# Kernel optimization log

Measured on AMD Instinct MI355X. Metric: run time of the kernel, lower is better.

## Reference

```python
import jax, jax.numpy as jnp
import numpy as np

N_NODES = 100000
N_EDGES = 1600000
IN_CH, OUT_CH = 6, 32


def _glorot(key, shape):
    fan_in, fan_out = shape[0], shape[1]
    lim = float(np.sqrt(6.0 / (fan_in + fan_out)))
    return jax.random.uniform(key, shape, jnp.float32, -lim, lim)


def setup_inputs() -> dict:
    key = jax.random.key(0)
    ks = jax.random.split(key, 16)
    x = jax.random.normal(ks[0], (N_NODES, IN_CH), jnp.float32)
    edge_tp = jax.random.randint(ks[1], (2, N_EDGES), 0, N_NODES, jnp.int32)
    edge_int = jax.random.randint(ks[2], (2, N_EDGES), 0, N_NODES, jnp.int32)
    return {
        'x': x, 'edge_tp': edge_tp, 'edge_int': edge_int,
        # block 1 (6 -> 32): self lin, per-edge-type message lins, residual proj
        'W_self1': _glorot(ks[3], (IN_CH, OUT_CH)), 'b1': jnp.zeros((OUT_CH,), jnp.float32),
        'W_tp1': _glorot(ks[4], (IN_CH, OUT_CH)), 'W_int1': _glorot(ks[5], (IN_CH, OUT_CH)),
        'W_res1': _glorot(ks[6], (IN_CH, OUT_CH)),
        # block 2 (32 -> 32): identity residual
        'W_self2': _glorot(ks[7], (OUT_CH, OUT_CH)), 'b2': jnp.zeros((OUT_CH,), jnp.float32),
        'W_tp2': _glorot(ks[8], (OUT_CH, OUT_CH)), 'W_int2': _glorot(ks[9], (OUT_CH, OUT_CH)),
        # instance decoder MLP
        'Wd1': _glorot(ks[10], (OUT_CH, OUT_CH)), 'bd1': jnp.zeros((OUT_CH,), jnp.float32),
        'Wd2': _glorot(ks[11], (OUT_CH, 1)), 'bd2': jnp.zeros((1,), jnp.float32),
    }


def _hetero_block(x, edge_tp, edge_int, W_self, b, W_tp, W_int, W_res):
    """One ResidualGeneralHeteroConvBlock: per-edge-type message passing
    ('temp_previous' -> sum-agg, 'intersects' -> mean-agg) + self transform +
    residual, then ReLU. x: [N, Cin]."""
    N = x.shape[0]
    # temp_previous: add reducer
    src, dst = edge_tp[0], edge_tp[1]
    m_tp = jax.ops.segment_sum(x[src] @ W_tp, dst, num_segments=N)  # [N, Cout]
    # intersects: mean reducer
    s2, d2 = edge_int[0], edge_int[1]
    m_sum = jax.ops.segment_sum(x[s2] @ W_int, d2, num_segments=N)
    cnt = jax.ops.segment_sum(jnp.ones(d2.shape, x.dtype), d2, num_segments=N)
    m_int = m_sum / jnp.maximum(cnt, 1.0)[:, None]
    res = x @ W_res if W_res is not None else x
    return jax.nn.relu(x @ W_self + b + m_tp + m_int + res)


def reference(x, edge_tp, edge_int,
              W_self1, b1, W_tp1, W_int1, W_res1,
              W_self2, b2, W_tp2, W_int2,
              Wd1, bd1, Wd2, bd2):
    h = _hetero_block(x, edge_tp, edge_int, W_self1, b1, W_tp1, W_int1, W_res1)
    h = _hetero_block(h, edge_tp, edge_int, W_self2, b2, W_tp2, W_int2, None)
    # instance decoder: Linear -> ReLU -> Linear -> sigmoid
    h = jax.nn.relu(h @ Wd1 + bd1)
    return jax.nn.sigmoid(h @ Wd2 + bd2)  # [N, 1]
```

## Files before the change

kernel.cpp:

```cpp
#include <hip/hip_runtime.h>
#include <hip/hip_bf16.h>
#include <math.h>

#define NN   100000
#define ICH  6
#define OCH  32
#define NBK  782
#define PBLK 256
#define CAPB 4720
#define CAPL 4800
#define GN   16
#define CHMAX 12500

#define WPREP_N 4480

typedef float f32x2 __attribute__((ext_vector_type(2)));
typedef float f32x4 __attribute__((ext_vector_type(4)));

__device__ __forceinline__ void pk_fma(f32x2& a, f32x2 x, f32x2 y) {
    asm("v_pk_fma_f32 %0, %1, %2, %0" : "+v"(a) : "v"(x), "v"(y));
}
__device__ __forceinline__ f32x2 pk_add(f32x2 x, f32x2 y) {
    f32x2 d;
    asm("v_pk_add_f32 %0, %1, %2" : "=v"(d) : "v"(x), "v"(y));
    return d;
}

__device__ __forceinline__ float ldf(const void* p, long i, int f32) {
    return f32 ? ((const float*)p)[i]
               : __bfloat162float(((const __hip_bfloat16*)p)[i]);
}
__device__ __forceinline__ float lo16f(unsigned u) { return __uint_as_float(u << 16); }
__device__ __forceinline__ float hi16f(unsigned u) { return __uint_as_float(u & 0xFFFF0000u); }

__device__ __forceinline__ int binof(int n, int s) {
    return ((n >> 7) << 8) | (s << 7) | (n & 127);
}

__global__ __launch_bounds__(1024) void partAx_r20(
        const int* __restrict__ src_tp, const int* __restrict__ dst_tp,
        const int* __restrict__ src_int, const int* __restrict__ dst_int,
        int Etp, int E,
        const void* __restrict__ x, unsigned* __restrict__ xw,
        int* __restrict__ gcnt, unsigned* __restrict__ part,
        int* __restrict__ flagp,
        const void* Ws2, const void* b2v, const void* Wt2, const void* Wi2,
        const void* Wd1, const void* bd1v, const void* Wd2, const void* bd2v,
        float* __restrict__ wprep) {
    __shared__ unsigned stage[CHMAX];
    __shared__ int lh[NBK];
    __shared__ int cur[NBK];
    __shared__ int lofs[NBK + 1];
    __shared__ int weird;
    int t = threadIdx.x, blk = blockIdx.x;
    if (t == 0) weird = 0;
    for (int b = t; b < NBK; b += 1024) lh[b] = 0;
    __syncthreads();
    {
        const __hip_bfloat16* p = (const __hip_bfloat16*)x;
        int w = 0;
        for (int i = t; i < 4096; i += 1024) {
            float v = fabsf(__bfloat162float(p[i]));
            if (!(v <= 1000.0f) || (v > 0.0f && v < 1e-4f)) w++;
        }
        if (w) atomicAdd(&weird, w);
    }
    __syncthreads();
    int f32 = (weird > 500) ? 1 : 0;
    if (blk == 0 && t == 0) *flagp = f32;
    if (blk == 0) {
        for (int i = t; i < 96 * 32; i += 1024) {
            int k = i >> 5, c = i & 31;
            float w;
            if (k < 32)      w = ldf(Ws2, k * 32 + c, f32) + ((k == c) ? 1.0f : 0.0f);
            else if (k < 64) w = ldf(Wt2, (k - 32) * 32 + c, f32);
            else             w = ldf(Wi2, (k - 64) * 32 + c, f32);
            wprep[c * 100 + k] = w;
        }
        for (int i = t; i < 32 * 32; i += 1024) {
            int k = i >> 5, c = i & 31;
            wprep[3200 + c * 36 + k] = ldf(Wd1, k * 32 + c, f32);
        }
        if (t < 32) {
            wprep[4352 + t]      = ldf(b2v, t, f32);
            wprep[4352 + 32 + t] = ldf(bd1v, t, f32);
            wprep[4352 + 64 + t] = ldf(Wd2, t, f32);
        }
        if (t == 0) wprep[4352 + 96] = ldf(bd2v, 0, f32);
    }
    for (int w = blk * 1024 + t; w < NN * 4; w += PBLK * 1024) {
        int n = w >> 2, j = w & 3;
        int c0 = 2 * j, c1 = 2 * j + 1;
        __hip_bfloat16 v0 = (c0 < ICH) ? __float2bfloat16(ldf(x, (long)n * ICH + c0, f32))
                                       : __float2bfloat16(0.0f);
        __hip_bfloat16 v1 = (c1 < ICH) ? __float2bfloat16(ldf(x, (long)n * ICH + c1, f32))
                                       : __float2bfloat16(0.0f);
        xw[w] = (unsigned)__bfloat16_as_ushort(v0) |
                ((unsigned)__bfloat16_as_ushort(v1) << 16);
    }
    int CH = (E + PBLK - 1) / PBLK;
    int lo = blk * CH, hi = min(E, lo + CH);
    int n = hi - lo;
    for (int e = lo + t; e < hi; e += 1024) {
        int bin = (e < Etp) ? binof(dst_tp[e], 0) : binof(dst_int[e - Etp], 1);
        atomicAdd(&lh[bin >> 8], 1);
    }
    __syncthreads();
    for (int b = t; b < NBK; b += 1024) {
        int cnt = lh[b];
        cur[b] = b * CAPB + (cnt ? atomicAdd(&gcnt[b], cnt) : 0);
    }
    {
        int* ss = (int*)stage;
        ss[t] = (t < NBK) ? lh[t] : 0;
        __syncthreads();
        for (int d = 1; d < 1024; d <<= 1) {
            int v = (t >= d) ? ss[t - d] : 0;
            __syncthreads();
            ss[t] += v;
            __syncthreads();
        }
        if (t < NBK) {
            int excl = ss[t] - lh[t];
            lofs[t] = excl;
            cur[t] -= excl;
            lh[t]  = excl;
        }
        if (t == 0) lofs[NBK] = n;
        __syncthreads();
    }
    for (int e = lo + t; e < hi; e += 1024) {
        int bin, src;
        if (e < Etp) { bin = binof(dst_tp[e], 0); src = src_tp[e]; }
        else         { bin = binof(dst_int[e - Etp], 1); src = src_int[e - Etp]; }
        int pos = atomicAdd(&lh[bin >> 8], 1);
        stage[pos] = ((unsigned)(bin & 255) << 24) | (unsigned)src;
    }
    __syncthreads();
    for (int i = t; i < n; i += 1024) {
        int blo = 0, bhi = NBK;
#pragma unroll
        for (int it = 0; it < 10; ++it) {
            int mid = (blo + bhi) >> 1;
            if (lofs[mid] <= i) blo = mid; else bhi = mid;
        }
        part[cur[blo] + i] = stage[i];
    }
}

__global__ __launch_bounds__(256) void passBn1_r20(
        unsigned* __restrict__ partcsr, const int* __restrict__ gcnt,
        int* __restrict__ off, int* __restrict__ end,
        const unsigned* __restrict__ xw,
        const void* Ws1, const void* b1v, const void* Wt1, const void* Wi1, const void* Wr1,
        unsigned* __restrict__ h1u, float* __restrict__ invc_a,
        const int* __restrict__ flag) {
    __shared__ unsigned lp[CAPL];
    __shared__ unsigned sorted[CAPL];
    __shared__ int scnt[256], sscan[256], obin[256];
    __shared__ float agg[256][7];
    __shared__ float sWs[ICH][32], sWt[ICH][32], sWi[ICH][32];
    __shared__ float sb1[32];
    int k = blockIdx.x, t = threadIdx.x;
    int f32 = *flag;
    if (k == 0 && t < 16) h1u[(size_t)NN * 16u + t] = 0u;
    if (t < ICH * OCH) {
        int kk = t >> 5, c = t & 31;
        sWs[kk][c] = ldf(Ws1, t, f32) + ldf(Wr1, t, f32);
        sWt[kk][c] = ldf(Wt1, t, f32);
        sWi[kk][c] = ldf(Wi1, t, f32);
    }
    if (t < 32) sb1[t] = ldf(b1v, t, f32);
    int s0 = k * CAPB;
    int cnt = gcnt[k]; if (cnt > CAPB) cnt = CAPB;
    scnt[t] = 0;
    __syncthreads();
    for (int i = t; i < cnt; i += 256) {
        unsigned v = partcsr[s0 + i];
        lp[i] = v;
        atomicAdd(&scnt[v >> 24], 1);
    }
    __syncthreads();
    int own = scnt[t];
    obin[t] = own;
    sscan[t] = own; __syncthreads();
    for (int d = 1; d < 256; d <<= 1) {
        int val = (t >= d) ? sscan[t - d] : 0;
        __syncthreads();
        sscan[t] += val;
        __syncthreads();
    }
    int excl = sscan[t] - own;
    scnt[t] = excl;
    off[k * 256 + t] = s0 + excl;
    end[k * 256 + t] = s0 + excl + own;
    __syncthreads();
    for (int i = t; i < cnt; i += 256) {
        unsigned v = lp[i];
        int pos = atomicAdd(&scnt[v >> 24], 1);
        sorted[pos] = v & 0xFFFFFFu;
    }
    __syncthreads();
    for (int i = t; i < cnt; i += 256) partcsr[s0 + i] = sorted[i];
    float a0 = 0, a1 = 0, a2 = 0, a3 = 0, a4 = 0, a5 = 0;
    {
        int i = excl, e = excl + own;
        for (; i + 4 <= e; i += 4) {
            unsigned q0 = sorted[i], q1 = sorted[i + 1];
            unsigned q2 = sorted[i + 2], q3 = sorted[i + 3];
            uint4 u0 = *(const uint4*)(xw + q0 * 4u);
            uint4 u1 = *(const uint4*)(xw + q1 * 4u);
            uint4 u2 = *(const uint4*)(xw + q2 * 4u);
            uint4 u3 = *(const uint4*)(xw + q3 * 4u);
            a0 += lo16f(u0.x) + lo16f(u1.x) + lo16f(u2.x) + lo16f(u3.x);
            a1 += hi16f(u0.x) + hi16f(u1.x) + hi16f(u2.x) + hi16f(u3.x);
            a2 += lo16f(u0.y) + lo16f(u1.y) + lo16f(u2.y) + lo16f(u3.y);
            a3 += hi16f(u0.y) + hi16f(u1.y) + hi16f(u2.y) + hi16f(u3.y);
            a4 += lo16f(u0.z) + lo16f(u1.z) + lo16f(u2.z) + lo16f(u3.z);
            a5 += hi16f(u0.z) + hi16f(u1.z) + hi16f(u2.z) + hi16f(u3.z);
        }
        for (; i < e; ++i) {
            uint4 u = *(const uint4*)(xw + sorted[i] * 4u);
            a0 += lo16f(u.x); a1 += hi16f(u.x);
            a2 += lo16f(u.y); a3 += hi16f(u.y);
            a4 += lo16f(u.z); a5 += hi16f(u.z);
        }
    }
    agg[t][0] = a0; agg[t][1] = a1; agg[t][2] = a2;
    agg[t][3] = a3; agg[t][4] = a4; agg[t][5] = a5;
    __syncthreads();

    int nl = t & 127, half = t >> 7;
    int node = k * 128 + nl;
    if (node < NN) {
        int degi = obin[128 + nl];
        float invc = 1.0f / fmaxf((float)degi, 1.0f);
        if (half == 0) invc_a[node] = invc;
        uint4 us = *(const uint4*)(xw + (unsigned)node * 4u);
        float xv[ICH] = {lo16f(us.x), hi16f(us.x), lo16f(us.y),
                         hi16f(us.y), lo16f(us.z), hi16f(us.z)};
        float aT[ICH], aI[ICH];
#pragma unroll
        for (int q = 0; q < ICH; ++q) {
            aT[q] = agg[nl][q];
            aI[q] = agg[128 + nl][q] * invc;
        }
        unsigned row[8];
#pragma unroll
        for (int cc = 0; cc < 8; ++cc) {
            int c0 = half * 16 + 2 * cc, c1 = c0 + 1;
            float v0 = sb1[c0], v1 = sb1[c1];
#pragma unroll
            for (int q = 0; q < ICH; ++q) {
                v0 += xv[q] * sWs[q][c0] + aT[q] * sWt[q][c0] + aI[q] * sWi[q][c0];
                v1 += xv[q] * sWs[q][c1] + aT[q] * sWt[q][c1] + aI[q] * sWi[q][c1];
            }
            unsigned w0 = (unsigned)__bfloat16_as_ushort(__float2bfloat16(fmaxf(v0, 0.0f)));
            unsigned w1 = (unsigned)__bfloat16_as_ushort(__float2bfloat16(fmaxf(v1, 0.0f)));
            row[cc] = w0 | (w1 << 16);
        }
        unsigned base = (unsigned)node * 16u + (unsigned)half * 8u;
        *(uint4*)(h1u + base)      = make_uint4(row[0], row[1], row[2], row[3]);
        *(uint4*)(h1u + base + 4u) = make_uint4(row[4], row[5], row[6], row[7]);
    }
}

__global__ __launch_bounds__(512, 8) void final_r20(
        const unsigned* __restrict__ h1u,
        const int* __restrict__ csr, const int* __restrict__ off,
        const int* __restrict__ end,
        const float* __restrict__ invc,
        const float* __restrict__ wprep,
        void* __restrict__ out, const int* __restrict__ flag) {
    __shared__ float wsh[WPREP_N];
    __shared__ float sv[GN][100];
    int t = threadIdx.x;
    int f32 = *flag;
    {
        const float4* wp4 = (const float4*)wprep;
        float4* ws4 = (float4*)wsh;
        for (int i = t; i < WPREP_N / 4; i += 512) ws4[i] = wp4[i];
    }
    __syncthreads();

    int g = t >> 5, c = t & 31;
    int sub = c >> 3, r = c & 7;
    int half = c >> 4, l = c & 15;
    int node = blockIdx.x * GN + g;

    unsigned uself = h1u[(unsigned)node * 16u + l];
    float ic = invc[node];
    int binA = ((node >> 7) << 8) | (node & 127);
    int binB = binA | 128;
    int sa0 = off[binA], sa1 = end[binA];
    int sb0 = off[binB], sb1_ = end[binB];
    int ma0 = sa1 - sa0; if (ma0 > 32) ma0 = 32;
    int mb0 = sb1_ - sb0; if (mb0 > 32) mb0 = 32;
    int idxa = (ma0 > 0) ? csr[sa0 + (c < ma0 ? c : ma0 - 1)] : 0;
    int idxb = (mb0 > 0) ? csr[sb0 + (c < mb0 ? c : mb0 - 1)] : 0;

    if (half == 0)
        *(float2*)&sv[g][2 * l] = make_float2(lo16f(uself), hi16f(uself));

#pragma unroll
    for (int set = 0; set < 2; ++set) {
        int s0 = set ? sb0 : sa0;
        int s1 = set ? sb1_ : sa1;
        int idx = set ? idxb : idxa;
        f32x2 v0 = {0.f, 0.f}, v1 = {0.f, 0.f};
        for (int base = s0; base < s1; base += 32) {
            int m = s1 - base; if (m > 32) m = 32;
            int nb = base + 32;
            int nm = s1 - nb; if (nm > 32) nm = 32;
            int nidx = (nm > 0) ? csr[nb + (c < nm ? c : nm - 1)] : 0;
            for (int b = 0; b < m; b += 16) {
                uint2 u[4];
#pragma unroll
                for (int q = 0; q < 4; ++q) {
                    int e = b + 4 * q + sub;
                    int sj = __shfl(idx, e & 31, 32);
                    sj = (e < m) ? sj : NN;
                    u[q] = *(const uint2*)(h1u + (unsigned)sj * 16u + 2u * r);
                }
#pragma unroll
                for (int q = 0; q < 4; ++q) {
                    f32x2 lx = {lo16f(u[q].x), hi16f(u[q].x)};
                    f32x2 ly = {lo16f(u[q].y), hi16f(u[q].y)};
                    v0 = pk_add(v0, lx);
                    v1 = pk_add(v1, ly);
                }
            }
            idx = nidx;
        }
#pragma unroll
        for (int sh = 8; sh <= 16; sh <<= 1) {
            v0.x += __shfl_down(v0.x, sh, 32);  v0.y += __shfl_down(v0.y, sh, 32);
            v1.x += __shfl_down(v1.x, sh, 32);  v1.y += __shfl_down(v1.y, sh, 32);
        }
        if (c < 8) {
            float sc = (set == 1) ? ic : 1.0f;
            *(float2*)&sv[g][32 + set * 32 + 4 * r]     = make_float2(v0.x * sc, v0.y * sc);
            *(float2*)&sv[g][32 + set * 32 + 4 * r + 2] = make_float2(v1.x * sc, v1.y * sc);
        }
    }

    const float* svg  = sv[g];
    const float* wrow = wsh + c * 100;
    f32x2 acc = {wsh[4352 + c], 0.f};
#pragma unroll 4
    for (int k = 0; k < 96; k += 4) {
        f32x4 s4 = *(const f32x4*)(svg + k);
        f32x4 w4 = *(const f32x4*)(wrow + k);
        pk_fma(acc, __builtin_shufflevector(s4, s4, 0, 1),
                    __builtin_shufflevector(w4, w4, 0, 1));
        pk_fma(acc, __builtin_shufflevector(s4, s4, 2, 3),
                    __builtin_shufflevector(w4, w4, 2, 3));
    }
    float h2 = fmaxf(acc.x + acc.y, 0.0f);
    sv[g][c] = h2;

    const float* wdrow = wsh + 3200 + c * 36;
    f32x2 acc2 = {wsh[4352 + 32 + c], 0.f};
#pragma unroll 4
    for (int k = 0; k < 32; k += 4) {
        f32x4 s4 = *(const f32x4*)(svg + k);
        f32x4 w4 = *(const f32x4*)(wdrow + k);
        pk_fma(acc2, __builtin_shufflevector(s4, s4, 0, 1),
                     __builtin_shufflevector(w4, w4, 0, 1));
        pk_fma(acc2, __builtin_shufflevector(s4, s4, 2, 3),
                     __builtin_shufflevector(w4, w4, 2, 3));
    }
    float h3 = fmaxf(acc2.x + acc2.y, 0.0f);

    float p = h3 * wsh[4352 + 64 + c];
#pragma unroll
    for (int offs = 16; offs; offs >>= 1) p += __shfl_down(p, offs, 32);
    if (c == 0) {
        float z = p + wsh[4352 + 96];
        float sgm = 1.0f / (1.0f + expf(-z));
        if (f32) ((float*)out)[node] = sgm;
        else     ((__hip_bfloat16*)out)[node] = __float2bfloat16(sgm);
    }
}

extern "C" void kernel_launch(void* const* d_in, const int* in_sizes, int n_in,
                              void* d_out, int out_size, void* d_ws, size_t ws_size,
                              hipStream_t stream) {
    const void* x      = d_in[0];
    const int* edge_tp = (const int*)d_in[1];
    const int* edge_int= (const int*)d_in[2];
    const void* Ws1 = d_in[3], *b1 = d_in[4], *Wt1 = d_in[5], *Wi1 = d_in[6], *Wr1 = d_in[7];
    const void* Ws2 = d_in[8], *b2 = d_in[9];
    const void* Wt2 = d_in[10], *Wi2 = d_in[11];
    const void* Wd1 = d_in[12], *bd1 = d_in[13], *Wd2 = d_in[14], *bd2 = d_in[15];

    const int E_tp  = in_sizes[1] / 2;
    const int E_int = in_sizes[2] / 2;

    int*      flag    = (int*)d_ws;
    int*      gcnt    = flag + 64;
    int*      off     = gcnt + 1024;
    int*      end     = off + 200448;
    unsigned* xw      = (unsigned*)(end + 200448);
    unsigned* partcsr = xw + (size_t)4 * NN;
    unsigned* h1u     = partcsr + (size_t)NBK * CAPB;
    float*    invc    = (float*)(h1u + (size_t)16 * (NN + 1));
    float*    wprep   = invc + NN;

    const int* src_tp  = edge_tp;
    const int* dst_tp  = edge_tp + E_tp;
    const int* src_int = edge_int;
    const int* dst_int = edge_int + E_int;

    hipMemsetAsync(gcnt, 0, NBK * sizeof(int), stream);

    partAx_r20<<<PBLK, 1024, 0, stream>>>(src_tp, dst_tp, src_int, dst_int,
                                          E_tp, E_tp + E_int, x, xw, gcnt,
                                          partcsr, flag,
                                          Ws2, b2, Wt2, Wi2, Wd1, bd1, Wd2, bd2,
                                          wprep);
    passBn1_r20<<<NBK, 256, 0, stream>>>(partcsr, gcnt, off, end, xw,
                                         Ws1, b1, Wt1, Wi1, Wr1,
                                         h1u, invc, flag);

    final_r20<<<NN / GN, 512, 0, stream>>>(h1u, (const int*)partcsr, off, end, invc,
                                           wprep, d_out, flag);
}
```

Before: 220.6 us.

## Interleave both edge-type gathers with 16-byte loads in final kernel

The final kernel's neighbour aggregation now processes the sum-aggregated and mean-aggregated edge lists in one fused loop instead of two sequential loops. Each lane gathers a uint4 (eight bf16 values) instead of a uint2, so eight neighbours are loaded per step. This puts more independent loads in flight per wave and halves the load instruction count. In exchange it uses more registers per thread (occupancy hint lowered from 8 to 6) and needs an extra shuffle-reduction stage. The fused loop also runs for the longer of the two lists.

```diff
diff --git a/kernel.cpp b/kernel.cpp
--- a/kernel.cpp
+++ b/kernel.cpp
@@ -37,7 +37,7 @@
     return ((n >> 7) << 8) | (s << 7) | (n & 127);
 }
 
-__global__ __launch_bounds__(1024) void partAx_r20(
+__global__ __launch_bounds__(1024) void partAx_r21(
         const int* __restrict__ src_tp, const int* __restrict__ dst_tp,
         const int* __restrict__ src_int, const int* __restrict__ dst_int,
         int Etp, int E,
@@ -148,7 +148,7 @@
     }
 }
 
-__global__ __launch_bounds__(256) void passBn1_r20(
+__global__ __launch_bounds__(256) void passBn1_r21(
         unsigned* __restrict__ partcsr, const int* __restrict__ gcnt,
         int* __restrict__ off, int* __restrict__ end,
         const unsigned* __restrict__ xw,
@@ -265,7 +265,7 @@
     }
 }
 
-__global__ __launch_bounds__(512, 8) void final_r20(
+__global__ __launch_bounds__(512, 6) void final_r21(
         const unsigned* __restrict__ h1u,
         const int* __restrict__ csr, const int* __restrict__ off,
         const int* __restrict__ end,
@@ -284,7 +284,7 @@
     __syncthreads();
 
     int g = t >> 5, c = t & 31;
-    int sub = c >> 3, r = c & 7;
+    int sub8 = c >> 2, r4 = c & 3;
     int half = c >> 4, l = c & 15;
     int node = blockIdx.x * GN + g;
 
@@ -296,52 +296,76 @@
     int sb0 = off[binB], sb1_ = end[binB];
     int ma0 = sa1 - sa0; if (ma0 > 32) ma0 = 32;
     int mb0 = sb1_ - sb0; if (mb0 > 32) mb0 = 32;
-    int idxa = (ma0 > 0) ? csr[sa0 + (c < ma0 ? c : ma0 - 1)] : 0;
-    int idxb = (mb0 > 0) ? csr[sb0 + (c < mb0 ? c : mb0 - 1)] : 0;
+    int idxA = (ma0 > 0) ? csr[sa0 + (c < ma0 ? c : ma0 - 1)] : 0;
+    int idxB = (mb0 > 0) ? csr[sb0 + (c < mb0 ? c : mb0 - 1)] : 0;
 
     if (half == 0)
         *(float2*)&sv[g][2 * l] = make_float2(lo16f(uself), hi16f(uself));
 
-#pragma unroll
-    for (int set = 0; set < 2; ++set) {
-        int s0 = set ? sb0 : sa0;
-        int s1 = set ? sb1_ : sa1;
-        int idx = set ? idxb : idxa;
-        f32x2 v0 = {0.f, 0.f}, v1 = {0.f, 0.f};
-        for (int base = s0; base < s1; base += 32) {
-            int m = s1 - base; if (m > 32) m = 32;
-            int nb = base + 32;
-            int nm = s1 - nb; if (nm > 32) nm = 32;
-            int nidx = (nm > 0) ? csr[nb + (c < nm ? c : nm - 1)] : 0;
-            for (int b = 0; b < m; b += 16) {
-                uint2 u[4];
-#pragma unroll
-                for (int q = 0; q < 4; ++q) {
-                    int e = b + 4 * q + sub;
-                    int sj = __shfl(idx, e & 31, 32);
-                    sj = (e < m) ? sj : NN;
-                    u[q] = *(const uint2*)(h1u + (unsigned)sj * 16u + 2u * r);
-                }
-#pragma unroll
-                for (int q = 0; q < 4; ++q) {
-                    f32x2 lx = {lo16f(u[q].x), hi16f(u[q].x)};
-                    f32x2 ly = {lo16f(u[q].y), hi16f(u[q].y)};
-                    v0 = pk_add(v0, lx);
-                    v1 = pk_add(v1, ly);
-                }
-            }
-            idx = nidx;
-        }
-#pragma unroll
-        for (int sh = 8; sh <= 16; sh <<= 1) {
-            v0.x += __shfl_down(v0.x, sh, 32);  v0.y += __shfl_down(v0.y, sh, 32);
-            v1.x += __shfl_down(v1.x, sh, 32);  v1.y += __shfl_down(v1.y, sh, 32);
-        }
-        if (c < 8) {
-            float sc = (set == 1) ? ic : 1.0f;
-            *(float2*)&sv[g][32 + set * 32 + 4 * r]     = make_float2(v0.x * sc, v0.y * sc);
-            *(float2*)&sv[g][32 + set * 32 + 4 * r + 2] = make_float2(v1.x * sc, v1.y * sc);
-        }
+    f32x2 va0 = {0.f, 0.f}, va1 = va0, va2 = va0, va3 = va0;
+    f32x2 vb0 = va0, vb1 = va0, vb2 = va0, vb3 = va0;
+    int sA = sa0, sB = sb0;
+    while (sA < sa1 || sB < sb1_) {
+        int mA = sa1 - sA; if (mA > 32) mA = 32;
+        int mB = sb1_ - sB; if (mB > 32) mB = 32;
+        int nA = sA + 32, nB = sB + 32;
+        int nmA = sa1 - nA; if (nmA > 32) nmA = 32;
+        int nmB = sb1_ - nB; if (nmB > 32) nmB = 32;
+        int nidxA = (nmA > 0) ? csr[nA + (c < nmA ? c : nmA - 1)] : 0;
+        int nidxB = (nmB > 0) ? csr[nB + (c < nmB ? c : nmB - 1)] : 0;
+        uint4 uA[4], uB[4];
+#pragma unroll
+        for (int q = 0; q < 4; ++q) {
+            int e = 8 * q + sub8;
+            int sj = __shfl(idxA, e, 32);
+            sj = (e < mA) ? sj : NN;
+            uA[q] = *(const uint4*)(h1u + (unsigned)sj * 16u + 4u * r4);
+        }
+#pragma unroll
+        for (int q = 0; q < 4; ++q) {
+            int e = 8 * q + sub8;
+            int sj = __shfl(idxB, e, 32);
+            sj = (e < mB) ? sj : NN;
+            uB[q] = *(const uint4*)(h1u + (unsigned)sj * 16u + 4u * r4);
+        }
+#pragma unroll
+        for (int q = 0; q < 4; ++q) {
+            f32x2 x0 = {lo16f(uA[q].x), hi16f(uA[q].x)};
+            f32x2 x1 = {lo16f(uA[q].y), hi16f(uA[q].y)};
+            f32x2 x2 = {lo16f(uA[q].z), hi16f(uA[q].z)};
+            f32x2 x3 = {lo16f(uA[q].w), hi16f(uA[q].w)};
+            va0 = pk_add(va0, x0); va1 = pk_add(va1, x1);
+            va2 = pk_add(va2, x2); va3 = pk_add(va3, x3);
+        }
+#pragma unroll
+        for (int q = 0; q < 4; ++q) {
+            f32x2 x0 = {lo16f(uB[q].x), hi16f(uB[q].x)};
+            f32x2 x1 = {lo16f(uB[q].y), hi16f(uB[q].y)};
+            f32x2 x2 = {lo16f(uB[q].z), hi16f(uB[q].z)};
+            f32x2 x3 = {lo16f(uB[q].w), hi16f(uB[q].w)};
+            vb0 = pk_add(vb0, x0); vb1 = pk_add(vb1, x1);
+            vb2 = pk_add(vb2, x2); vb3 = pk_add(vb3, x3);
+        }
+        idxA = nidxA; idxB = nidxB; sA = nA; sB = nB;
+    }
+#pragma unroll
+    for (int sh = 4; sh <= 16; sh <<= 1) {
+        va0.x += __shfl_down(va0.x, sh, 32); va0.y += __shfl_down(va0.y, sh, 32);
+        va1.x += __shfl_down(va1.x, sh, 32); va1.y += __shfl_down(va1.y, sh, 32);
+        va2.x += __shfl_down(va2.x, sh, 32); va2.y += __shfl_down(va2.y, sh, 32);
+        va3.x += __shfl_down(va3.x, sh, 32); va3.y += __shfl_down(va3.y, sh, 32);
+        vb0.x += __shfl_down(vb0.x, sh, 32); vb0.y += __shfl_down(vb0.y, sh, 32);
+        vb1.x += __shfl_down(vb1.x, sh, 32); vb1.y += __shfl_down(vb1.y, sh, 32);
+        vb2.x += __shfl_down(vb2.x, sh, 32); vb2.y += __shfl_down(vb2.y, sh, 32);
+        vb3.x += __shfl_down(vb3.x, sh, 32); vb3.y += __shfl_down(vb3.y, sh, 32);
+    }
+    if (c < 4) {
+        *(float4*)&sv[g][32 + 8 * r4]     = make_float4(va0.x, va0.y, va1.x, va1.y);
+        *(float4*)&sv[g][32 + 8 * r4 + 4] = make_float4(va2.x, va2.y, va3.x, va3.y);
+        *(float4*)&sv[g][64 + 8 * r4]     = make_float4(vb0.x * ic, vb0.y * ic,
+                                                        vb1.x * ic, vb1.y * ic);
+        *(float4*)&sv[g][64 + 8 * r4 + 4] = make_float4(vb2.x * ic, vb2.y * ic,
+                                                        vb3.x * ic, vb3.y * ic);
     }
 
     const float* svg  = sv[g];
@@ -414,15 +438,15 @@
 
     hipMemsetAsync(gcnt, 0, NBK * sizeof(int), stream);
 
-    partAx_r20<<<PBLK, 1024, 0, stream>>>(src_tp, dst_tp, src_int, dst_int,
+    partAx_r21<<<PBLK, 1024, 0, stream>>>(src_tp, dst_tp, src_int, dst_int,
                                           E_tp, E_tp + E_int, x, xw, gcnt,
                                           partcsr, flag,
                                           Ws2, b2, Wt2, Wi2, Wd1, bd1, Wd2, bd2,
                                           wprep);
-    passBn1_r20<<<NBK, 256, 0, stream>>>(partcsr, gcnt, off, end, xw,
+    passBn1_r21<<<NBK, 256, 0, stream>>>(partcsr, gcnt, off, end, xw,
                                          Ws1, b1, Wt1, Wi1, Wr1,
                                          h1u, invc, flag);
 
-    final_r20<<<NN / GN, 512, 0, stream>>>(h1u, (const int*)partcsr, off, end, invc,
+    final_r21<<<NN / GN, 512, 0, stream>>>(h1u, (const int*)partcsr, off, end, invc,
                                            wprep, d_out, flag);
 }
```

Result: slower. 243.8 us (+10.6%).
